# Optimization experiments

Measured on AMD Instinct MI355X. Metric: run time of the kernel, lower is better.

## Reference

```python
import jax, jax.numpy as jnp
import numpy as np

BZ, SRC_LEN, TGT_LEN, DIM = 32, 1024, 1024, 512


def setup_inputs() -> dict:
    key = jax.random.key(0)
    k1, k2, k3, k4 = jax.random.split(key, 4)
    src = jax.random.normal(k1, (BZ, SRC_LEN, DIM), dtype=jnp.float32)
    tgt = jax.random.normal(k2, (BZ, TGT_LEN, DIM), dtype=jnp.float32)
    # lengths in [1, SRC_LEN] so every row has at least one valid position
    src_lengths = jax.random.randint(k3, (BZ,), 1, SRC_LEN + 1, dtype=jnp.int64)
    # nn.Linear(2*dim, dim, bias=False): weight shape (dim, 2*dim)
    bound = 1.0 / np.sqrt(2 * DIM)
    w_out = jax.random.uniform(k4, (DIM, 2 * DIM), dtype=jnp.float32,
                               minval=-bound, maxval=bound)
    return {"src": src, "tgt": tgt, "src_lengths": src_lengths, "w_out": w_out}


def reference(src, tgt, src_lengths, w_out):
    # dot-product attention scores: (bz, tgt_len, src_len)
    score = jnp.einsum("btd,bsd->bts", tgt, src)
    # mask out padded source positions (position >= length)
    valid = jnp.arange(src.shape[1])[None, :] < src_lengths[:, None]  # (bz, src_len)
    score = jnp.where(valid[:, None, :], score, -jnp.inf)
    align = jax.nn.softmax(score, axis=-1)
    # context: (bz, tgt_len, dim)
    c = jnp.einsum("bts,bsd->btd", align, src)
    concat_c = jnp.concatenate([c, tgt], axis=-1)  # (bz, tgt_len, 2*dim)
    attn_h = jnp.einsum("bte,de->btd", concat_c, w_out)
    return attn_h, align
```

## Files before the change

### kernel.cpp

```cpp
#include <hip/hip_runtime.h>
#include <hip/hip_bf16.h>

typedef __attribute__((ext_vector_type(4))) float  f32x4;
typedef __attribute__((ext_vector_type(4))) float  float4v;
typedef __attribute__((ext_vector_type(8))) short  bf16x8;
typedef __attribute__((ext_vector_type(4))) short  bf16x4;

#define BZ   32
#define SLEN 1024
#define TLEN 1024
#define DIM  512
#define TILE 128
#define LP   40

__device__ __forceinline__ unsigned short f2bf(float x) {
  union { float f; unsigned int u; } v; v.f = x;
  unsigned int r = v.u + 0x7FFFu + ((v.u >> 16) & 1u);
  return (unsigned short)(r >> 16);
}
__device__ __forceinline__ float bf2f(unsigned short h) {
  union { float f; unsigned int u; } v; v.u = ((unsigned int)h) << 16;
  return v.f;
}
__device__ __forceinline__ int get_len(const int* __restrict__ p, int b) {
  bool is64 = (p[1] == 0) && (p[3] == 0) && (p[5] == 0);
  return is64 ? p[2 * b] : p[b];
}

#define TLP 68
__global__ __launch_bounds__(256) void k_transpose(
    const float* __restrict__ src, unsigned short* __restrict__ srcT) {
  const int b  = blockIdx.z;
  const int s0 = blockIdx.x * 64;
  const int d0 = blockIdx.y * 64;
  __shared__ unsigned short tl[64 * TLP];
  const int tid = threadIdx.x;
#pragma unroll
  for (int r = 0; r < 4; ++r) {
    const int idx = tid + 256 * r;
    const int row = idx >> 4, c4 = idx & 15;
    float4v x = *(const float4v*)(src + ((size_t)(b * SLEN + s0 + row)) * DIM + d0 + c4 * 4);
    unsigned short* pp = tl + row * TLP + c4 * 4;
    pp[0] = f2bf(x[0]); pp[1] = f2bf(x[1]); pp[2] = f2bf(x[2]); pp[3] = f2bf(x[3]);
  }
  __syncthreads();
#pragma unroll
  for (int r = 0; r < 2; ++r) {
    const int idx  = tid + 256 * r;
    const int drow = idx >> 3, c8 = idx & 7;
    union { unsigned short u[8]; bf16x8 v; } pk;
#pragma unroll
    for (int j = 0; j < 8; ++j) pk.u[j] = tl[(c8 * 8 + j) * TLP + drow];
    *(bf16x8*)(srcT + ((size_t)(b * DIM + d0 + drow)) * SLEN + s0 + c8 * 8) = pk.v;
  }
}

__global__ __launch_bounds__(256) void k_score(
    const float* __restrict__ tgt, const float* __restrict__ src,
    const int* __restrict__ lens, float* __restrict__ align_out) {
  const int b  = blockIdx.z;
  const int t0 = blockIdx.x * TILE;
  const int s0 = blockIdx.y * TILE;
  const int len = get_len(lens, b);
  if (s0 >= len) return;

  __shared__ short aHi[TILE * LP], aLo[TILE * LP], bHi[TILE * LP], bLo[TILE * LP];

  const int tid  = threadIdx.x;
  const int lane = tid & 63;
  const int wid  = tid >> 6;
  const int wt   = wid >> 1, wsd = wid & 1;
  const int g    = lane >> 4, r16 = lane & 15;

  f32x4 acc[4][4];
#pragma unroll
  for (int m = 0; m < 4; ++m)
#pragma unroll
    for (int n = 0; n < 4; ++n) acc[m][n] = (f32x4){0.f, 0.f, 0.f, 0.f};

  const float* tgtB = tgt + ((size_t)(b * TLEN + t0)) * DIM;
  const float* srcB = src + ((size_t)(b * SLEN + s0)) * DIM;
  const int srow = tid >> 3, sc4 = tid & 7;

  for (int k0 = 0; k0 < DIM; k0 += 32) {
#pragma unroll
    for (int r = 0; r < 4; ++r) {
      const int row = srow + 32 * r;
      float4v va = *(const float4v*)(tgtB + (size_t)row * DIM + k0 + sc4 * 4);
      float4v vb = *(const float4v*)(srcB + (size_t)row * DIM + k0 + sc4 * 4);
      bf16x4 ah, al, bh, bl;
#pragma unroll
      for (int j = 0; j < 4; ++j) {
        unsigned short h = f2bf(va[j]);
        ah[j] = (short)h; al[j] = (short)f2bf(va[j] - bf2f(h));
        unsigned short h2 = f2bf(vb[j]);
        bh[j] = (short)h2; bl[j] = (short)f2bf(vb[j] - bf2f(h2));
      }
      const int o = row * LP + sc4 * 4;
      *(bf16x4*)(aHi + o) = ah; *(bf16x4*)(aLo + o) = al;
      *(bf16x4*)(bHi + o) = bh; *(bf16x4*)(bLo + o) = bl;
    }
    __syncthreads();
    bf16x8 fah[4], fal[4], fbh[4], fbl[4];
#pragma unroll
    for (int m = 0; m < 4; ++m) {
      const int row = wt * 64 + m * 16 + r16;
      fah[m] = *(const bf16x8*)(aHi + row * LP + g * 8);
      fal[m] = *(const bf16x8*)(aLo + row * LP + g * 8);
    }
#pragma unroll
    for (int n = 0; n < 4; ++n) {
      const int row = wsd * 64 + n * 16 + r16;
      fbh[n] = *(const bf16x8*)(bHi + row * LP + g * 8);
      fbl[n] = *(const bf16x8*)(bLo + row * LP + g * 8);
    }
#pragma unroll
    for (int m = 0; m < 4; ++m)
#pragma unroll
      for (int n = 0; n < 4; ++n) {
        acc[m][n] = __builtin_amdgcn_mfma_f32_16x16x32_bf16(fah[m], fbh[n], acc[m][n], 0, 0, 0);
        acc[m][n] = __builtin_amdgcn_mfma_f32_16x16x32_bf16(fal[m], fbh[n], acc[m][n], 0, 0, 0);
        acc[m][n] = __builtin_amdgcn_mfma_f32_16x16x32_bf16(fah[m], fbl[n], acc[m][n], 0, 0, 0);
      }
    __syncthreads();
  }
  float* outB = align_out + ((size_t)(b * TLEN + t0)) * SLEN + s0;
#pragma unroll
  for (int m = 0; m < 4; ++m) {
    const int tr = wt * 64 + m * 16 + g * 4;
#pragma unroll
    for (int n = 0; n < 4; ++n) {
      const int sc = wsd * 64 + n * 16 + r16;
#pragma unroll
      for (int r = 0; r < 4; ++r)
        outB[(size_t)(tr + r) * SLEN + sc] = acc[m][n][r];
    }
  }
}

__global__ __launch_bounds__(256) void k_softmax(
    const int* __restrict__ lens, float* __restrict__ align_io) {
  const int row  = blockIdx.x * 4 + (threadIdx.x >> 6);
  const int lane = threadIdx.x & 63;
  const int b    = row >> 10;
  const int len  = get_len(lens, b);
  float* p = align_io + (size_t)row * SLEN;
  float v[4][4];
  float mx = -3.0e38f;
#pragma unroll
  for (int q = 0; q < 4; ++q) {
    const int sb = (lane + 64 * q) * 4;
    float4v x = *(const float4v*)(p + sb);
#pragma unroll
    for (int j = 0; j < 4; ++j) {
      v[q][j] = x[j];
      if (sb + j < len) mx = fmaxf(mx, x[j]);
    }
  }
#pragma unroll
  for (int off = 1; off < 64; off <<= 1) mx = fmaxf(mx, __shfl_xor(mx, off));
  float sum = 0.f;
#pragma unroll
  for (int q = 0; q < 4; ++q) {
    const int sb = (lane + 64 * q) * 4;
#pragma unroll
    for (int j = 0; j < 4; ++j) {
      float e = (sb + j < len) ? __expf(v[q][j] - mx) : 0.f;
      v[q][j] = e; sum += e;
    }
  }
#pragma unroll
  for (int off = 1; off < 64; off <<= 1) sum += __shfl_xor(sum, off);
  const float inv = 1.f / sum;
#pragma unroll
  for (int q = 0; q < 4; ++q) {
    float4v x;
#pragma unroll
    for (int j = 0; j < 4; ++j) x[j] = v[q][j] * inv;
    *(float4v*)(p + (lane + 64 * q) * 4) = x;
  }
}

__global__ __launch_bounds__(256) void k_pv(
    const float* __restrict__ align_in, const unsigned short* __restrict__ srcT,
    const int* __restrict__ lens, unsigned short* __restrict__ cws) {
  const int b  = blockIdx.z;
  const int t0 = blockIdx.x * TILE;
  const int d0 = blockIdx.y * TILE;
  const int len = get_len(lens, b);
  const int ksteps = (len + 31) >> 5;

  __shared__ short A[TILE * LP], B[TILE * LP];
  const int tid  = threadIdx.x;
  const int lane = tid & 63;
  const int wid  = tid >> 6;
  const int wt   = wid >> 1, wsd = wid & 1;
  const int g    = lane >> 4, r16 = lane & 15;

  f32x4 acc[4][4];
#pragma unroll
  for (int m = 0; m < 4; ++m)
#pragma unroll
    for (int n = 0; n < 4; ++n) acc[m][n] = (f32x4){0.f, 0.f, 0.f, 0.f};

  for (int ks = 0; ks < ksteps; ++ks) {
    const int k0 = ks * 32;
#pragma unroll
    for (int r = 0; r < 4; ++r) {
      const int row = (tid >> 3) + 32 * r, c4 = tid & 7;
      float4v x = *(const float4v*)(align_in + ((size_t)(b * TLEN + t0 + row)) * SLEN + k0 + c4 * 4);
      bf16x4 h;
#pragma unroll
      for (int j = 0; j < 4; ++j) h[j] = (short)f2bf(x[j]);
      *(bf16x4*)(A + row * LP + c4 * 4) = h;
    }
#pragma unroll
    for (int r = 0; r < 2; ++r) {
      const int row = (tid >> 2) + 64 * r, c8 = tid & 3;
      bf16x8 x = *(const bf16x8*)(srcT + ((size_t)(b * DIM + d0 + row)) * SLEN + k0 + c8 * 8);
      *(bf16x8*)(B + row * LP + c8 * 8) = x;
    }
    __syncthreads();
    bf16x8 fa[4], fb[4];
#pragma unroll
    for (int m = 0; m < 4; ++m) fa[m] = *(const bf16x8*)(A + (wt * 64 + m * 16 + r16) * LP + g * 8);
#pragma unroll
    for (int n = 0; n < 4; ++n) fb[n] = *(const bf16x8*)(B + (wsd * 64 + n * 16 + r16) * LP + g * 8);
#pragma unroll
    for (int m = 0; m < 4; ++m)
#pragma unroll
      for (int n = 0; n < 4; ++n)
        acc[m][n] = __builtin_amdgcn_mfma_f32_16x16x32_bf16(fa[m], fb[n], acc[m][n], 0, 0, 0);
    __syncthreads();
  }
#pragma unroll
  for (int m = 0; m < 4; ++m) {
    const int tr = wt * 64 + m * 16 + g * 4;
#pragma unroll
    for (int n = 0; n < 4; ++n) {
      const int dc = wsd * 64 + n * 16 + r16;
#pragma unroll
      for (int r = 0; r < 4; ++r)
        cws[((size_t)(b * TLEN + t0 + tr + r)) * DIM + d0 + dc] = f2bf(acc[m][n][r]);
    }
  }
}

__global__ __launch_bounds__(256) void k_proj(
    const unsigned short* __restrict__ cws, const float* __restrict__ tgt,
    const float* __restrict__ w_out, float* __restrict__ attn_out) {
  const int b  = blockIdx.z;
  const int t0 = blockIdx.x * TILE;
  const int d0 = blockIdx.y * TILE;

  __shared__ short A[TILE * LP], B[TILE * LP];
  const int tid  = threadIdx.x;
  const int lane = tid & 63;
  const int wid  = tid >> 6;
  const int wt   = wid >> 1, wsd = wid & 1;
  const int g    = lane >> 4, r16 = lane & 15;

  f32x4 acc[4][4];
#pragma unroll
  for (int m = 0; m < 4; ++m)
#pragma unroll
    for (int n = 0; n < 4; ++n) acc[m][n] = (f32x4){0.f, 0.f, 0.f, 0.f};

  for (int k0 = 0; k0 < 2 * DIM; k0 += 32) {
    if (k0 < DIM) {
#pragma unroll
      for (int r = 0; r < 2; ++r) {
        const int row = (tid >> 2) + 64 * r, c8 = tid & 3;
        bf16x8 x = *(const bf16x8*)(cws + ((size_t)(b * TLEN + t0 + row)) * DIM + k0 + c8 * 8);
        *(bf16x8*)(A + row * LP + c8 * 8) = x;
      }
    } else {
#pragma unroll
      for (int r = 0; r < 4; ++r) {
        const int row = (tid >> 3) + 32 * r, c4 = tid & 7;
        float4v x = *(const float4v*)(tgt + ((size_t)(b * TLEN + t0 + row)) * DIM + (k0 - DIM) + c4 * 4);
        bf16x4 h;
#pragma unroll
        for (int j = 0; j < 4; ++j) h[j] = (short)f2bf(x[j]);
        *(bf16x4*)(A + row * LP + c4 * 4) = h;
      }
    }
#pragma unroll
    for (int r = 0; r < 4; ++r) {
      const int row = (tid >> 3) + 32 * r, c4 = tid & 7;
      float4v x = *(const float4v*)(w_out + ((size_t)(d0 + row)) * (2 * DIM) + k0 + c4 * 4);
      bf16x4 h;
#pragma unroll
      for (int j = 0; j < 4; ++j) h[j] = (short)f2bf(x[j]);
      *(bf16x4*)(B + row * LP + c4 * 4) = h;
    }
    __syncthreads();
    bf16x8 fa[4], fb[4];
#pragma unroll
    for (int m = 0; m < 4; ++m) fa[m] = *(const bf16x8*)(A + (wt * 64 + m * 16 + r16) * LP + g * 8);
#pragma unroll
    for (int n = 0; n < 4; ++n) fb[n] = *(const bf16x8*)(B + (wsd * 64 + n * 16 + r16) * LP + g * 8);
#pragma unroll
    for (int m = 0; m < 4; ++m)
#pragma unroll
      for (int n = 0; n < 4; ++n)
        acc[m][n] = __builtin_amdgcn_mfma_f32_16x16x32_bf16(fa[m], fb[n], acc[m][n], 0, 0, 0);
    __syncthreads();
  }
#pragma unroll
  for (int m = 0; m < 4; ++m) {
    const int tr = wt * 64 + m * 16 + g * 4;
#pragma unroll
    for (int n = 0; n < 4; ++n) {
      const int dc = wsd * 64 + n * 16 + r16;
#pragma unroll
      for (int r = 0; r < 4; ++r)
        attn_out[((size_t)(b * TLEN + t0 + tr + r)) * DIM + d0 + dc] = acc[m][n][r];
    }
  }
}

extern "C" void kernel_launch(void* const* d_in, const int* in_sizes, int n_in,
                              void* d_out, int out_size, void* d_ws, size_t ws_size,
                              hipStream_t stream) {
  const float* src   = (const float*)d_in[0];
  const float* tgt   = (const float*)d_in[1];
  const int*   lens  = (const int*)d_in[2];
  const float* w_out = (const float*)d_in[3];

  float* attn_out  = (float*)d_out;
  float* align_out = attn_out + (size_t)BZ * TLEN * DIM;

  unsigned short* srcT = (unsigned short*)d_ws;
  unsigned short* cws  = srcT + (size_t)BZ * DIM * SLEN;

  k_transpose<<<dim3(16, 8, BZ), 256, 0, stream>>>(src, srcT);
  k_score<<<dim3(8, 8, BZ), 256, 0, stream>>>(tgt, src, lens, align_out);
  k_softmax<<<dim3(BZ * TLEN / 4), 256, 0, stream>>>(lens, align_out);
  k_pv<<<dim3(8, 4, BZ), 256, 0, stream>>>(align_out, srcT, lens, cws);
  k_proj<<<dim3(8, 4, BZ), 256, 0, stream>>>(cws, tgt, w_out, attn_out);
}
```

Baseline: 301.3 us.

## Precompute bf16 hi/lo splits of src, tgt and weights in prep kernels

Adds prep kernels that convert src, tgt and w_out to bf16, with hi/lo split pairs for the score GEMM, and stores them in workspace. The score and projection kernels then load ready-made bf16 tiles instead of re-converting fp32 data in every tile, which was redundant across the many blocks that reread the same rows. A tier system picks the path based on how much workspace is available. In exchange it adds extra global writes and reads of the split arrays and more kernel launches.

New measurement: 333.2 us. 10.6% more time.

```diff
diff --git a/kernel.cpp b/kernel.cpp
--- a/kernel.cpp
+++ b/kernel.cpp
@@ -28,20 +28,35 @@
 }
 
 #define TLP 68
-__global__ __launch_bounds__(256) void k_transpose(
-    const float* __restrict__ src, unsigned short* __restrict__ srcT) {
+template<bool PB>
+__global__ __launch_bounds__(256) void k_prep_src(
+    const float* __restrict__ src, unsigned short* __restrict__ srcT,
+    unsigned short* __restrict__ srcHi, unsigned short* __restrict__ srcLo) {
   const int b  = blockIdx.z;
   const int s0 = blockIdx.x * 64;
   const int d0 = blockIdx.y * 64;
   __shared__ unsigned short tl[64 * TLP];
   const int tid = threadIdx.x;
 #pragma unroll
-  for (int r = 0; r < 4; ++r) {
+  for (int r = 0; r < 2; ++r) {
     const int idx = tid + 256 * r;
-    const int row = idx >> 4, c4 = idx & 15;
-    float4v x = *(const float4v*)(src + ((size_t)(b * SLEN + s0 + row)) * DIM + d0 + c4 * 4);
-    unsigned short* pp = tl + row * TLP + c4 * 4;
-    pp[0] = f2bf(x[0]); pp[1] = f2bf(x[1]); pp[2] = f2bf(x[2]); pp[3] = f2bf(x[3]);
+    const int row = idx >> 3, c8 = idx & 7;
+    const size_t goff = ((size_t)(b * SLEN + s0 + row)) * DIM + d0 + c8 * 8;
+    float4v x0 = *(const float4v*)(src + goff);
+    float4v x1 = *(const float4v*)(src + goff + 4);
+    union { unsigned short u[8]; bf16x8 v; } hi, lo;
+#pragma unroll
+    for (int j = 0; j < 4; ++j) {
+      unsigned short h0 = f2bf(x0[j]);
+      hi.u[j] = h0; lo.u[j] = f2bf(x0[j] - bf2f(h0));
+      unsigned short h1 = f2bf(x1[j]);
+      hi.u[4 + j] = h1; lo.u[4 + j] = f2bf(x1[j] - bf2f(h1));
+    }
+    *(bf16x8*)(tl + row * TLP + c8 * 8) = hi.v;
+    if constexpr (PB) {
+      *(bf16x8*)(srcHi + goff) = hi.v;
+      *(bf16x8*)(srcLo + goff) = lo.v;
+    }
   }
   __syncthreads();
 #pragma unroll
@@ -55,8 +70,41 @@
   }
 }
 
+__global__ __launch_bounds__(256) void k_prep_tgt(
+    const float* __restrict__ tgt, unsigned short* __restrict__ hi_out,
+    unsigned short* __restrict__ lo_out) {
+  const size_t i = ((size_t)blockIdx.x * 256 + threadIdx.x) * 8;
+  float4v x0 = *(const float4v*)(tgt + i);
+  float4v x1 = *(const float4v*)(tgt + i + 4);
+  union { unsigned short u[8]; bf16x8 v; } hi, lo;
+#pragma unroll
+  for (int j = 0; j < 4; ++j) {
+    unsigned short h0 = f2bf(x0[j]);
+    hi.u[j] = h0; lo.u[j] = f2bf(x0[j] - bf2f(h0));
+    unsigned short h1 = f2bf(x1[j]);
+    hi.u[4 + j] = h1; lo.u[4 + j] = f2bf(x1[j] - bf2f(h1));
+  }
+  *(bf16x8*)(hi_out + i) = hi.v;
+  *(bf16x8*)(lo_out + i) = lo.v;
+}
+
+__global__ __launch_bounds__(256) void k_prep_w(
+    const float* __restrict__ w, unsigned short* __restrict__ wbf) {
+  const size_t i = ((size_t)blockIdx.x * 256 + threadIdx.x) * 8;
+  float4v x0 = *(const float4v*)(w + i);
+  float4v x1 = *(const float4v*)(w + i + 4);
+  union { unsigned short u[8]; bf16x8 v; } hi;
+#pragma unroll
+  for (int j = 0; j < 4; ++j) { hi.u[j] = f2bf(x0[j]); hi.u[4 + j] = f2bf(x1[j]); }
+  *(bf16x8*)(wbf + i) = hi.v;
+}
+
+template<bool PA, bool PB>
 __global__ __launch_bounds__(256) void k_score(
-    const float* __restrict__ tgt, const float* __restrict__ src,
+    const float* __restrict__ tgt, const unsigned short* __restrict__ tgtHi,
+    const unsigned short* __restrict__ tgtLo,
+    const float* __restrict__ src, const unsigned short* __restrict__ srcHi,
+    const unsigned short* __restrict__ srcLo,
     const int* __restrict__ lens, float* __restrict__ align_out) {
   const int b  = blockIdx.z;
   const int t0 = blockIdx.x * TILE;
@@ -78,27 +126,55 @@
 #pragma unroll
     for (int n = 0; n < 4; ++n) acc[m][n] = (f32x4){0.f, 0.f, 0.f, 0.f};
 
-  const float* tgtB = tgt + ((size_t)(b * TLEN + t0)) * DIM;
-  const float* srcB = src + ((size_t)(b * SLEN + s0)) * DIM;
-  const int srow = tid >> 3, sc4 = tid & 7;
+  const size_t aBase = ((size_t)(b * TLEN + t0)) * DIM;
+  const size_t bBase = ((size_t)(b * SLEN + s0)) * DIM;
 
   for (int k0 = 0; k0 < DIM; k0 += 32) {
-#pragma unroll
-    for (int r = 0; r < 4; ++r) {
-      const int row = srow + 32 * r;
-      float4v va = *(const float4v*)(tgtB + (size_t)row * DIM + k0 + sc4 * 4);
-      float4v vb = *(const float4v*)(srcB + (size_t)row * DIM + k0 + sc4 * 4);
-      bf16x4 ah, al, bh, bl;
-#pragma unroll
-      for (int j = 0; j < 4; ++j) {
-        unsigned short h = f2bf(va[j]);
-        ah[j] = (short)h; al[j] = (short)f2bf(va[j] - bf2f(h));
-        unsigned short h2 = f2bf(vb[j]);
-        bh[j] = (short)h2; bl[j] = (short)f2bf(vb[j] - bf2f(h2));
-      }
-      const int o = row * LP + sc4 * 4;
-      *(bf16x4*)(aHi + o) = ah; *(bf16x4*)(aLo + o) = al;
-      *(bf16x4*)(bHi + o) = bh; *(bf16x4*)(bLo + o) = bl;
+    if constexpr (PA) {
+#pragma unroll
+      for (int r = 0; r < 2; ++r) {
+        const int row = (tid >> 2) + 64 * r, c8 = tid & 3;
+        const size_t o = aBase + (size_t)row * DIM + k0 + c8 * 8;
+        *(bf16x8*)(aHi + row * LP + c8 * 8) = *(const bf16x8*)(tgtHi + o);
+        *(bf16x8*)(aLo + row * LP + c8 * 8) = *(const bf16x8*)(tgtLo + o);
+      }
+    } else {
+#pragma unroll
+      for (int r = 0; r < 4; ++r) {
+        const int row = (tid >> 3) + 32 * r, c4 = tid & 7;
+        float4v va = *(const float4v*)(tgt + aBase + (size_t)row * DIM + k0 + c4 * 4);
+        bf16x4 ah, al;
+#pragma unroll
+        for (int j = 0; j < 4; ++j) {
+          unsigned short h = f2bf(va[j]);
+          ah[j] = (short)h; al[j] = (short)f2bf(va[j] - bf2f(h));
+        }
+        const int o = row * LP + c4 * 4;
+        *(bf16x4*)(aHi + o) = ah; *(bf16x4*)(aLo + o) = al;
+      }
+    }
+    if constexpr (PB) {
+#pragma unroll
+      for (int r = 0; r < 2; ++r) {
+        const int row = (tid >> 2) + 64 * r, c8 = tid & 3;
+        const size_t o = bBase + (size_t)row * DIM + k0 + c8 * 8;
+        *(bf16x8*)(bHi + row * LP + c8 * 8) = *(const bf16x8*)(srcHi + o);
+        *(bf16x8*)(bLo + row * LP + c8 * 8) = *(const bf16x8*)(srcLo + o);
+      }
+    } else {
+#pragma unroll
+      for (int r = 0; r < 4; ++r) {
+        const int row = (tid >> 3) + 32 * r, c4 = tid & 7;
+        float4v vb = *(const float4v*)(src + bBase + (size_t)row * DIM + k0 + c4 * 4);
+        bf16x4 bh, bl;
+#pragma unroll
+        for (int j = 0; j < 4; ++j) {
+          unsigned short h2 = f2bf(vb[j]);
+          bh[j] = (short)h2; bl[j] = (short)f2bf(vb[j] - bf2f(h2));
+        }
+        const int o = row * LP + c4 * 4;
+        *(bf16x4*)(bHi + o) = bh; *(bf16x4*)(bLo + o) = bl;
+      }
     }
     __syncthreads();
     bf16x8 fah[4], fal[4], fbh[4], fbl[4];
@@ -246,9 +322,11 @@
   }
 }
 
+template<bool PT>
 __global__ __launch_bounds__(256) void k_proj(
     const unsigned short* __restrict__ cws, const float* __restrict__ tgt,
-    const float* __restrict__ w_out, float* __restrict__ attn_out) {
+    const unsigned short* __restrict__ tgtHi, const unsigned short* __restrict__ wbf,
+    float* __restrict__ attn_out) {
   const int b  = blockIdx.z;
   const int t0 = blockIdx.x * TILE;
   const int d0 = blockIdx.y * TILE;
@@ -274,6 +352,13 @@
         bf16x8 x = *(const bf16x8*)(cws + ((size_t)(b * TLEN + t0 + row)) * DIM + k0 + c8 * 8);
         *(bf16x8*)(A + row * LP + c8 * 8) = x;
       }
+    } else if constexpr (PT) {
+#pragma unroll
+      for (int r = 0; r < 2; ++r) {
+        const int row = (tid >> 2) + 64 * r, c8 = tid & 3;
+        bf16x8 x = *(const bf16x8*)(tgtHi + ((size_t)(b * TLEN + t0 + row)) * DIM + (k0 - DIM) + c8 * 8);
+        *(bf16x8*)(A + row * LP + c8 * 8) = x;
+      }
     } else {
 #pragma unroll
       for (int r = 0; r < 4; ++r) {
@@ -286,13 +371,10 @@
       }
     }
 #pragma unroll
-    for (int r = 0; r < 4; ++r) {
-      const int row = (tid >> 3) + 32 * r, c4 = tid & 7;
-      float4v x = *(const float4v*)(w_out + ((size_t)(d0 + row)) * (2 * DIM) + k0 + c4 * 4);
-      bf16x4 h;
-#pragma unroll
-      for (int j = 0; j < 4; ++j) h[j] = (short)f2bf(x[j]);
-      *(bf16x4*)(B + row * LP + c4 * 4) = h;
+    for (int r = 0; r < 2; ++r) {
+      const int row = (tid >> 2) + 64 * r, c8 = tid & 3;
+      bf16x8 x = *(const bf16x8*)(wbf + ((size_t)(d0 + row)) * (2 * DIM) + k0 + c8 * 8);
+      *(bf16x8*)(B + row * LP + c8 * 8) = x;
     }
     __syncthreads();
     bf16x8 fa[4], fb[4];
@@ -331,12 +413,41 @@
   float* attn_out  = (float*)d_out;
   float* align_out = attn_out + (size_t)BZ * TLEN * DIM;
 
-  unsigned short* srcT = (unsigned short*)d_ws;
-  unsigned short* cws  = srcT + (size_t)BZ * DIM * SLEN;
-
-  k_transpose<<<dim3(16, 8, BZ), 256, 0, stream>>>(src, srcT);
-  k_score<<<dim3(8, 8, BZ), 256, 0, stream>>>(tgt, src, lens, align_out);
+  const size_t NE = (size_t)BZ * SLEN * DIM;
+  const size_t NW = (size_t)DIM * 2 * DIM;
+  unsigned short* srcT  = (unsigned short*)d_ws;
+  unsigned short* cws   = srcT + NE;
+  unsigned short* wbf   = cws + NE;
+  unsigned short* srcHi = wbf + NW;
+  unsigned short* srcLo = srcHi + NE;
+  unsigned short* tgtHi = srcLo + NE;
+  unsigned short* tgtLo = tgtHi + NE;
+
+  const size_t need1 = (size_t)((char*)(tgtHi)      - (char*)d_ws);
+  const size_t need2 = (size_t)((char*)(tgtLo + NE) - (char*)d_ws);
+  const int tier = (ws_size >= need2) ? 2 : (ws_size >= need1 ? 1 : 0);
+
+  if (tier >= 1)
+    k_prep_src<true ><<<dim3(16, 8, BZ), 256, 0, stream>>>(src, srcT, srcHi, srcLo);
+  else
+    k_prep_src<false><<<dim3(16, 8, BZ), 256, 0, stream>>>(src, srcT, srcHi, srcLo);
+
+  if (tier == 2)
+    k_prep_tgt<<<dim3((unsigned)(BZ * TLEN * DIM / 8 / 256)), 256, 0, stream>>>(tgt, tgtHi, tgtLo);
+  k_prep_w<<<dim3((unsigned)(NW / 8 / 256)), 256, 0, stream>>>(w_out, wbf);
+
+  if (tier == 2)
+    k_score<true , true ><<<dim3(8, 8, BZ), 256, 0, stream>>>(tgt, tgtHi, tgtLo, src, srcHi, srcLo, lens, align_out);
+  else if (tier == 1)
+    k_score<false, true ><<<dim3(8, 8, BZ), 256, 0, stream>>>(tgt, tgtHi, tgtLo, src, srcHi, srcLo, lens, align_out);
+  else
+    k_score<false, false><<<dim3(8, 8, BZ), 256, 0, stream>>>(tgt, tgtHi, tgtLo, src, srcHi, srcLo, lens, align_out);
+
   k_softmax<<<dim3(BZ * TLEN / 4), 256, 0, stream>>>(lens, align_out);
   k_pv<<<dim3(8, 4, BZ), 256, 0, stream>>>(align_out, srcT, lens, cws);
-  k_proj<<<dim3(8, 4, BZ), 256, 0, stream>>>(cws, tgt, w_out, attn_out);
-}
+
+  if (tier == 2)
+    k_proj<true ><<<dim3(8, 4, BZ), 256, 0, stream>>>(cws, tgt, tgtHi, wbf, attn_out);
+  else
+    k_proj<false><<<dim3(8, 4, BZ), 256, 0, stream>>>(cws, tgt, tgtHi, wbf, attn_out);
+}
```
